# Performance work log

Hardware: AMD Instinct MI355X
Metric: run time of the kernel (lower is better)

## Reference

```python
import jax, jax.numpy as jnp
import numpy as np

B, LQ, LK, D = 16, 2048, 2048, 256
NEG = -1e10


def setup_inputs() -> dict:
    key = jax.random.key(0)
    k1, k2, k3, k4, k5 = jax.random.split(key, 5)
    scale = 1.0 / np.sqrt(D)
    return {
        "x": jax.random.normal(k1, (B, LQ, D), dtype=jnp.float32),
        "y": jax.random.normal(k2, (B, LK, D), dtype=jnp.float32),
        "mask": jnp.zeros((B, LK), dtype=bool),  # True = padded key position
        "Wq": jax.random.normal(k3, (D, D), dtype=jnp.float32) * scale,
        "Wk": jax.random.normal(k4, (D, D), dtype=jnp.float32) * scale,
        "Wv": jax.random.normal(k5, (D, D), dtype=jnp.float32) * scale,
    }


def reference(x, y, mask, Wq, Wk, Wv):
    # nn.Linear: out = in @ W.T (no bias)
    q = jnp.einsum('bqd,ed->bqe', x, Wq)   # [B, LQ, D]
    k = jnp.einsum('bkd,ed->bke', y, Wk)   # [B, LK, D]
    v = jnp.einsum('bkd,ed->bke', y, Wv)   # [B, LK, D]
    # cdist (p=2) via GEMM expansion: ||q||^2 + ||k||^2 - 2 q.k
    qn = jnp.sum(q * q, axis=-1)                              # [B, LQ]
    kn = jnp.sum(k * k, axis=-1)                              # [B, LK]
    d2 = qn[:, :, None] + kn[:, None, :] - 2.0 * jnp.einsum('bqd,bkd->bqk', q, k)
    dist = jnp.sqrt(jnp.maximum(d2, 0.0))                     # [B, LQ, LK]
    scores = jnp.exp(-dist)
    # masked_fill: where original mask is True, set pre-softmax score to -1e10
    scores = jnp.where(mask[:, None, :], NEG, scores)
    attn = jax.nn.softmax(scores, axis=-1)                    # [B, LQ, LK]
    att_out = jnp.einsum('bqk,bkd->bqd', attn, v)             # [B, LQ, D]
    return (att_out, attn)
```

## Files before the change

### kernel.cpp

```cpp
#include <hip/hip_runtime.h>
#include <stdint.h>

#define B_   16
#define L_   2048
#define D_   256
#define NROW (B_*L_)

#define KPAD 264
#define VPAD 40
#define EPAD 40
#define TPAD 66

typedef __attribute__((ext_vector_type(8))) short s8v;
typedef __attribute__((ext_vector_type(4))) float f4v;

__device__ __forceinline__ unsigned short f2b(float f) {
    unsigned u = __builtin_bit_cast(unsigned, f);
    return (unsigned short)((u + 0x7fffu + ((u >> 16) & 1u)) >> 16);
}

__global__ __launch_bounds__(256) void qkv_kernel(
    const float* __restrict__ x, const float* __restrict__ y,
    const float* __restrict__ Wq, const float* __restrict__ Wk, const float* __restrict__ Wv,
    unsigned short* __restrict__ Qb, unsigned short* __restrict__ Kb,
    unsigned short* __restrict__ Vt,
    float* __restrict__ qn, float* __restrict__ kn)
{
    __shared__ unsigned short Xs[64*256];
    __shared__ unsigned short Ws[64*256];
    __shared__ unsigned short Ts[64*TPAD];

    const int t    = threadIdx.x;
    const int r0   = blockIdx.x * 64;
    const int type = blockIdx.y;

    const float* X = (type == 0) ? x : y;
    const float* W = (type == 0) ? Wq : (type == 1) ? Wk : Wv;

    #pragma unroll
    for (int p = 0; p < 16; ++p) {
        int idx = p*256 + t;
        int row = idx >> 6;
        int c4  = (idx & 63) * 4;
        float4 vx = *(const float4*)(X + (size_t)(r0+row)*D_ + c4);
        uint2 px;
        px.x = (unsigned)f2b(vx.x) | ((unsigned)f2b(vx.y) << 16);
        px.y = (unsigned)f2b(vx.z) | ((unsigned)f2b(vx.w) << 16);
        *(uint2*)(Xs + row*256 + c4) = px;
    }

    const int w = t >> 6, lane = t & 63, q16 = lane & 15, quad = lane >> 4;
    const int m0 = w * 16;

    float p4[4] = {0.f, 0.f, 0.f, 0.f};
    const f4v z4 = {0.f, 0.f, 0.f, 0.f};

    for (int ct = 0; ct < 4; ++ct) {
        const int e0 = ct * 64;
        __syncthreads();
        #pragma unroll
        for (int p = 0; p < 16; ++p) {
            int idx = p*256 + t;
            int row = idx >> 6;
            int c4  = (idx & 63) * 4;
            float4 vw = *(const float4*)(W + (size_t)(e0+row)*D_ + c4);
            uint2 pw;
            pw.x = (unsigned)f2b(vw.x) | ((unsigned)f2b(vw.y) << 16);
            pw.y = (unsigned)f2b(vw.z) | ((unsigned)f2b(vw.w) << 16);
            *(uint2*)(Ws + row*256 + c4) = pw;
        }
        __syncthreads();

        f4v acc[4];
        #pragma unroll
        for (int n = 0; n < 4; ++n) acc[n] = z4;

        #pragma unroll
        for (int c = 0; c < 8; ++c) {
            s8v a = *(const s8v*)(Xs + (m0 + q16)*256 + c*32 + quad*8);
            #pragma unroll
            for (int n = 0; n < 4; ++n) {
                s8v bb = *(const s8v*)(Ws + (n*16 + q16)*256 + c*32 + quad*8);
                acc[n] = __builtin_amdgcn_mfma_f32_16x16x32_bf16(a, bb, acc[n], 0, 0, 0);
            }
        }

        if (type < 2) {
            unsigned short* Out = (type == 0) ? Qb : Kb;
            #pragma unroll
            for (int n = 0; n < 4; ++n)
                #pragma unroll
                for (int r = 0; r < 4; ++r) {
                    float v = acc[n][r];
                    p4[r] += v * v;
                    Out[(size_t)(r0 + m0 + quad*4 + r)*D_ + e0 + n*16 + q16] = f2b(v);
                }
        } else {
            #pragma unroll
            for (int n = 0; n < 4; ++n)
                #pragma unroll
                for (int r = 0; r < 4; ++r)
                    Ts[(m0 + quad*4 + r)*TPAD + n*16 + q16] = f2b(acc[n][r]);
            __syncthreads();
            int j    = t >> 2;
            int kseg = t & 3;
            unsigned pk[8];
            #pragma unroll
            for (int i = 0; i < 8; ++i) {
                unsigned lo = Ts[(kseg*16 + 2*i    )*TPAD + j];
                unsigned hi = Ts[(kseg*16 + 2*i + 1)*TPAD + j];
                pk[i] = lo | (hi << 16);
            }
            int bb_ = r0 >> 11;
            int k0g = r0 & (L_ - 1);
            unsigned short* dst = Vt + (size_t)(bb_*D_ + e0 + j)*L_ + k0g + kseg*16;
            *(uint4*)dst       = make_uint4(pk[0], pk[1], pk[2], pk[3]);
            *((uint4*)dst + 1) = make_uint4(pk[4], pk[5], pk[6], pk[7]);
        }
    }

    if (type < 2) {
        float* norm = (type == 0) ? qn : kn;
        #pragma unroll
        for (int r = 0; r < 4; ++r) {
            float v = p4[r];
            v += __shfl_xor(v, 1, 16);
            v += __shfl_xor(v, 2, 16);
            v += __shfl_xor(v, 4, 16);
            v += __shfl_xor(v, 8, 16);
            if (q16 == 0) norm[r0 + m0 + quad*4 + r] = v;
        }
    }
}

__global__ __launch_bounds__(256) void attn_kernel(
    const unsigned short* __restrict__ Qb, const unsigned short* __restrict__ Kb,
    const unsigned short* __restrict__ Vt,
    const float* __restrict__ qn, const float* __restrict__ kn,
    const unsigned char* __restrict__ mask,
    float* __restrict__ attn_out, float* __restrict__ att_out)
{
    __shared__ unsigned short Ks[32*KPAD];
    __shared__ unsigned short Vs[256*VPAD];
    __shared__ unsigned short Es[4][16*EPAD];
    __shared__ float kns[32];
    __shared__ unsigned char ms[2048];

    const int t  = threadIdx.x;
    const int q0 = blockIdx.x * 64;
    const int b  = blockIdx.y;
    const int bk = b * L_;
    const int w = t >> 6, lane = t & 63, q16 = lane & 15, quad = lane >> 4;

    *(unsigned long long*)(ms + t*8) = *(const unsigned long long*)(mask + bk + t*8);

    const int qrow = bk + q0 + w*16;
    s8v qa[8];
    float qnr[4];
    #pragma unroll
    for (int c = 0; c < 8; ++c)
        qa[c] = *(const s8v*)(Qb + (size_t)(qrow + q16)*D_ + c*32 + quad*8);
    #pragma unroll
    for (int r = 0; r < 4; ++r)
        qnr[r] = qn[qrow + quad*4 + r];

    float rs[4] = {};

    for (int kt = 0; kt < 64; ++kt) {
        int k0 = kt * 32;
        #pragma unroll
        for (int p = 0; p < 4; ++p) {
            int idx = p*256 + t;
            int row = idx >> 5;
            int c8  = (idx & 31) * 8;
            *(uint4*)(Ks + row*KPAD + c8) =
                *(const uint4*)(Kb + (size_t)(bk + k0 + row)*D_ + c8);
        }
        if (t < 32) kns[t] = kn[bk + k0 + t];
        __syncthreads();
        #pragma unroll
        for (int n = 0; n < 2; ++n) {
            f4v s = {0.f, 0.f, 0.f, 0.f};
            #pragma unroll
            for (int c = 0; c < 8; ++c) {
                s8v bb = *(const s8v*)(Ks + (n*16 + q16)*KPAD + c*32 + quad*8);
                s = __builtin_amdgcn_mfma_f32_16x16x32_bf16(qa[c], bb, s, 0, 0, 0);
            }
            float kc = kns[n*16 + q16];
            bool mk = ms[k0 + n*16 + q16] != 0;
            #pragma unroll
            for (int r = 0; r < 4; ++r) {
                float d2 = qnr[r] + kc - 2.0f * s[r];
                float dist = sqrtf(fmaxf(d2, 0.f));
                rs[r] += mk ? 0.f : __expf(__expf(-dist));
            }
        }
        __syncthreads();
    }

    float inv[4];
    #pragma unroll
    for (int r = 0; r < 4; ++r) {
        float v = rs[r];
        v += __shfl_xor(v, 1, 16);
        v += __shfl_xor(v, 2, 16);
        v += __shfl_xor(v, 4, 16);
        v += __shfl_xor(v, 8, 16);
        inv[r] = 1.0f / v;
    }

    const f4v z4 = {0.f, 0.f, 0.f, 0.f};
    f4v O[16];
    #pragma unroll
    for (int n = 0; n < 16; ++n) O[n] = z4;

    for (int kt = 0; kt < 64; ++kt) {
        int k0 = kt * 32;
        #pragma unroll
        for (int p = 0; p < 4; ++p) {
            int idx = p*256 + t;
            int row = idx >> 5;
            int c8  = (idx & 31) * 8;
            *(uint4*)(Ks + row*KPAD + c8) =
                *(const uint4*)(Kb + (size_t)(bk + k0 + row)*D_ + c8);
        }
        #pragma unroll
        for (int p = 0; p < 4; ++p) {
            int idx = p*256 + t;
            int d   = idx >> 2;
            int seg = (idx & 3) * 8;
            *(uint4*)(Vs + d*VPAD + seg) =
                *(const uint4*)(Vt + (size_t)(b*D_ + d)*L_ + k0 + seg);
        }
        if (t < 32) kns[t] = kn[bk + k0 + t];
        __syncthreads();

        #pragma unroll
        for (int n = 0; n < 2; ++n) {
            f4v s = {0.f, 0.f, 0.f, 0.f};
            #pragma unroll
            for (int c = 0; c < 8; ++c) {
                s8v bb = *(const s8v*)(Ks + (n*16 + q16)*KPAD + c*32 + quad*8);
                s = __builtin_amdgcn_mfma_f32_16x16x32_bf16(qa[c], bb, s, 0, 0, 0);
            }
            float kc = kns[n*16 + q16];
            bool mk = ms[k0 + n*16 + q16] != 0;
            #pragma unroll
            for (int r = 0; r < 4; ++r) {
                float d2 = qnr[r] + kc - 2.0f * s[r];
                float dist = sqrtf(fmaxf(d2, 0.f));
                float E = mk ? 0.f : __expf(__expf(-dist));
                float av = E * inv[r];
                attn_out[(size_t)(qrow + quad*4 + r)*L_ + k0 + n*16 + q16] = av;
                Es[w][(quad*4 + r)*EPAD + n*16 + q16] = f2b(av);
            }
        }
        s8v af = *(const s8v*)(&Es[w][q16*EPAD + quad*8]);
        #pragma unroll
        for (int n = 0; n < 16; ++n) {
            s8v vb = *(const s8v*)(Vs + (n*16 + q16)*VPAD + quad*8);
            O[n] = __builtin_amdgcn_mfma_f32_16x16x32_bf16(af, vb, O[n], 0, 0, 0);
        }
        __syncthreads();
    }

    #pragma unroll
    for (int n = 0; n < 16; ++n)
        #pragma unroll
        for (int r = 0; r < 4; ++r)
            att_out[(size_t)(qrow + quad*4 + r)*D_ + n*16 + q16] = O[n][r];
}

extern "C" void kernel_launch(void* const* d_in, const int* in_sizes, int n_in,
                              void* d_out, int out_size, void* d_ws, size_t ws_size,
                              hipStream_t stream) {
    (void)in_sizes; (void)n_in; (void)out_size; (void)ws_size;
    const float* x  = (const float*)d_in[0];
    const float* y  = (const float*)d_in[1];
    const unsigned char* mask = (const unsigned char*)d_in[2];
    const float* Wq = (const float*)d_in[3];
    const float* Wk = (const float*)d_in[4];
    const float* Wv = (const float*)d_in[5];

    char* ws = (char*)d_ws;
    unsigned short* Qb = (unsigned short*)ws;
    unsigned short* Kb = Qb + (size_t)NROW * D_;
    unsigned short* Vt = Kb + (size_t)NROW * D_;
    float* qn = (float*)(ws + 3 * (size_t)NROW * D_ * 2);
    float* kn = qn + NROW;

    float* att_out = (float*)d_out;
    float* attn    = att_out + (size_t)NROW * D_;

    qkv_kernel<<<dim3(512, 3), 256, 0, stream>>>(x, y, Wq, Wk, Wv,
                                                 Qb, Kb, Vt, qn, kn);
    attn_kernel<<<dim3(32, 16), 256, 0, stream>>>(Qb, Kb, Vt, qn, kn, mask,
                                                  attn, att_out);
}
```

Baseline: 635.6 us.

## Split attention into rowsum and output kernels with async double-buffered LDS staging

```diff
diff --git a/kernel.cpp b/kernel.cpp
--- a/kernel.cpp
+++ b/kernel.cpp
@@ -6,8 +6,6 @@
 #define D_   256
 #define NROW (B_*L_)
 
-#define KPAD 264
-#define VPAD 40
 #define EPAD 40
 #define TPAD 66
 
@@ -17,6 +15,12 @@
 __device__ __forceinline__ unsigned short f2b(float f) {
     unsigned u = __builtin_bit_cast(unsigned, f);
     return (unsigned short)((u + 0x7fffu + ((u >> 16) & 1u)) >> 16);
+}
+
+__device__ __forceinline__ void gl16(const void* g, void* l) {
+    __builtin_amdgcn_global_load_lds(
+        (const __attribute__((address_space(1))) unsigned int*)g,
+        (__attribute__((address_space(3))) unsigned int*)l, 16, 0, 0);
 }
 
 __global__ __launch_bounds__(256) void qkv_kernel(
@@ -34,19 +38,20 @@
     const int r0   = blockIdx.x * 64;
     const int type = blockIdx.y;
 
-    const float* X = (type == 0) ? x : y;
-    const float* W = (type == 0) ? Wq : (type == 1) ? Wk : Wv;
+    const float* X = type ? y : x;
 
     #pragma unroll
     for (int p = 0; p < 16; ++p) {
-        int idx = p*256 + t;
-        int row = idx >> 6;
-        int c4  = (idx & 63) * 4;
+        int idx  = p*256 + t;
+        int row  = idx >> 6;
+        int half = idx & 1;
+        int blk  = (idx & 63) >> 1;
+        int c4   = blk*8 + half*4;
         float4 vx = *(const float4*)(X + (size_t)(r0+row)*D_ + c4);
         uint2 px;
         px.x = (unsigned)f2b(vx.x) | ((unsigned)f2b(vx.y) << 16);
         px.y = (unsigned)f2b(vx.z) | ((unsigned)f2b(vx.w) << 16);
-        *(uint2*)(Xs + row*256 + c4) = px;
+        *(uint2*)(Xs + row*256 + (blk ^ (row & 15))*8 + half*4) = px;
     }
 
     const int w = t >> 6, lane = t & 63, q16 = lane & 15, quad = lane >> 4;
@@ -57,36 +62,40 @@
 
     for (int ct = 0; ct < 4; ++ct) {
         const int e0 = ct * 64;
+
         __syncthreads();
-        #pragma unroll
-        for (int p = 0; p < 16; ++p) {
-            int idx = p*256 + t;
-            int row = idx >> 6;
-            int c4  = (idx & 63) * 4;
-            float4 vw = *(const float4*)(W + (size_t)(e0+row)*D_ + c4);
-            uint2 pw;
-            pw.x = (unsigned)f2b(vw.x) | ((unsigned)f2b(vw.y) << 16);
-            pw.y = (unsigned)f2b(vw.z) | ((unsigned)f2b(vw.w) << 16);
-            *(uint2*)(Ws + row*256 + c4) = pw;
+        {
+            const float* W = type ? Wk : Wq;
+            #pragma unroll
+            for (int p = 0; p < 16; ++p) {
+                int idx  = p*256 + t;
+                int row  = idx >> 6;
+                int half = idx & 1;
+                int blk  = (idx & 63) >> 1;
+                int c4   = blk*8 + half*4;
+                float4 vw = *(const float4*)(W + (size_t)(e0+row)*D_ + c4);
+                uint2 pw;
+                pw.x = (unsigned)f2b(vw.x) | ((unsigned)f2b(vw.y) << 16);
+                pw.y = (unsigned)f2b(vw.z) | ((unsigned)f2b(vw.w) << 16);
+                *(uint2*)(Ws + row*256 + (blk ^ (row & 15))*8 + half*4) = pw;
+            }
         }
         __syncthreads();
 
         f4v acc[4];
         #pragma unroll
         for (int n = 0; n < 4; ++n) acc[n] = z4;
-
         #pragma unroll
         for (int c = 0; c < 8; ++c) {
-            s8v a = *(const s8v*)(Xs + (m0 + q16)*256 + c*32 + quad*8);
+            s8v a = *(const s8v*)(Xs + (m0 + q16)*256 + (((c*4+quad) ^ q16)*8));
             #pragma unroll
             for (int n = 0; n < 4; ++n) {
-                s8v bb = *(const s8v*)(Ws + (n*16 + q16)*256 + c*32 + quad*8);
+                s8v bb = *(const s8v*)(Ws + (n*16 + q16)*256 + (((c*4+quad) ^ q16)*8));
                 acc[n] = __builtin_amdgcn_mfma_f32_16x16x32_bf16(a, bb, acc[n], 0, 0, 0);
             }
         }
-
-        if (type < 2) {
-            unsigned short* Out = (type == 0) ? Qb : Kb;
+        {
+            unsigned short* Out = type ? Kb : Qb;
             #pragma unroll
             for (int n = 0; n < 4; ++n)
                 #pragma unroll
@@ -95,12 +104,42 @@
                     p4[r] += v * v;
                     Out[(size_t)(r0 + m0 + quad*4 + r)*D_ + e0 + n*16 + q16] = f2b(v);
                 }
-        } else {
+        }
+
+        if (type) {
+            __syncthreads();
+            #pragma unroll
+            for (int p = 0; p < 16; ++p) {
+                int idx  = p*256 + t;
+                int row  = idx >> 6;
+                int half = idx & 1;
+                int blk  = (idx & 63) >> 1;
+                int c4   = blk*8 + half*4;
+                float4 vw = *(const float4*)(Wv + (size_t)(e0+row)*D_ + c4);
+                uint2 pw;
+                pw.x = (unsigned)f2b(vw.x) | ((unsigned)f2b(vw.y) << 16);
+                pw.y = (unsigned)f2b(vw.z) | ((unsigned)f2b(vw.w) << 16);
+                *(uint2*)(Ws + row*256 + (blk ^ (row & 15))*8 + half*4) = pw;
+            }
+            __syncthreads();
+
+            f4v vacc[4];
+            #pragma unroll
+            for (int n = 0; n < 4; ++n) vacc[n] = z4;
+            #pragma unroll
+            for (int c = 0; c < 8; ++c) {
+                s8v a = *(const s8v*)(Xs + (m0 + q16)*256 + (((c*4+quad) ^ q16)*8));
+                #pragma unroll
+                for (int n = 0; n < 4; ++n) {
+                    s8v bb = *(const s8v*)(Ws + (n*16 + q16)*256 + (((c*4+quad) ^ q16)*8));
+                    vacc[n] = __builtin_amdgcn_mfma_f32_16x16x32_bf16(a, bb, vacc[n], 0, 0, 0);
+                }
+            }
             #pragma unroll
             for (int n = 0; n < 4; ++n)
                 #pragma unroll
                 for (int r = 0; r < 4; ++r)
-                    Ts[(m0 + quad*4 + r)*TPAD + n*16 + q16] = f2b(acc[n][r]);
+                    Ts[(m0 + quad*4 + r)*TPAD + n*16 + q16] = f2b(vacc[n][r]);
             __syncthreads();
             int j    = t >> 2;
             int kseg = t & 3;
@@ -119,8 +158,8 @@
         }
     }
 
-    if (type < 2) {
-        float* norm = (type == 0) ? qn : kn;
+    {
+        float* norm = type ? kn : qn;
         #pragma unroll
         for (int r = 0; r < 4; ++r) {
             float v = p4[r];
@@ -133,26 +172,43 @@
     }
 }
 
-__global__ __launch_bounds__(256) void attn_kernel(
+__device__ __forceinline__ void stage_K(const unsigned short* Kb, unsigned short* ks,
+                                        int bk, int k0, int w, int lane) {
+    #pragma unroll
+    for (int p = 0; p < 4; ++p) {
+        int slot = p*256 + w*64 + lane;
+        int row  = slot >> 5;
+        int blk  = slot & 31;
+        gl16(Kb + (size_t)(bk + k0 + row)*D_ + ((blk ^ (row & 15))*8),
+             ks + (size_t)(p*256 + w*64)*8);
+    }
+}
+__device__ __forceinline__ void stage_V(const unsigned short* Vt, unsigned short* vs,
+                                        int bD, int k0, int w, int lane) {
+    #pragma unroll
+    for (int p = 0; p < 4; ++p) {
+        int slot = p*256 + w*64 + lane;
+        int d    = slot >> 2;
+        int blk  = slot & 3;
+        gl16(Vt + (size_t)(bD + d)*L_ + k0 + ((blk ^ ((d >> 1) & 3))*8),
+             vs + (size_t)(p*256 + w*64)*8);
+    }
+}
+
+__global__ __launch_bounds__(256) void rowsum_kernel(
     const unsigned short* __restrict__ Qb, const unsigned short* __restrict__ Kb,
-    const unsigned short* __restrict__ Vt,
     const float* __restrict__ qn, const float* __restrict__ kn,
     const unsigned char* __restrict__ mask,
-    float* __restrict__ attn_out, float* __restrict__ att_out)
+    float* __restrict__ rowsum)
 {
-    __shared__ unsigned short Ks[32*KPAD];
-    __shared__ unsigned short Vs[256*VPAD];
-    __shared__ unsigned short Es[4][16*EPAD];
-    __shared__ float kns[32];
-    __shared__ unsigned char ms[2048];
+    __shared__ unsigned short Ks[2][32*256];
 
     const int t  = threadIdx.x;
     const int q0 = blockIdx.x * 64;
     const int b  = blockIdx.y;
     const int bk = b * L_;
+    const int kbase = blockIdx.z * 1024;
     const int w = t >> 6, lane = t & 63, q16 = lane & 15, quad = lane >> 4;
-
-    *(unsigned long long*)(ms + t*8) = *(const unsigned long long*)(mask + bk + t*8);
 
     const int qrow = bk + q0 + w*16;
     s8v qa[8];
@@ -164,41 +220,38 @@
     for (int r = 0; r < 4; ++r)
         qnr[r] = qn[qrow + quad*4 + r];
 
-    float rs[4] = {};
-
-    for (int kt = 0; kt < 64; ++kt) {
-        int k0 = kt * 32;
-        #pragma unroll
-        for (int p = 0; p < 4; ++p) {
-            int idx = p*256 + t;
-            int row = idx >> 5;
-            int c8  = (idx & 31) * 8;
-            *(uint4*)(Ks + row*KPAD + c8) =
-                *(const uint4*)(Kb + (size_t)(bk + k0 + row)*D_ + c8);
-        }
-        if (t < 32) kns[t] = kn[bk + k0 + t];
+    float rs[4] = {0.f, 0.f, 0.f, 0.f};
+
+    stage_K(Kb, Ks[0], bk, kbase, w, lane);
+    for (int kt = 0; kt < 32; ++kt) {
+        const int k0 = kbase + kt*32;
+        const int cur = kt & 1;
         __syncthreads();
+        if (kt < 31) stage_K(Kb, Ks[cur ^ 1], bk, k0 + 32, w, lane);
+
+        float kcv[2]; int mkv[2];
+        #pragma unroll
+        for (int n = 0; n < 2; ++n) {
+            kcv[n] = kn[bk + k0 + n*16 + q16];
+            mkv[n] = mask[bk + k0 + n*16 + q16];
+        }
         #pragma unroll
         for (int n = 0; n < 2; ++n) {
             f4v s = {0.f, 0.f, 0.f, 0.f};
             #pragma unroll
             for (int c = 0; c < 8; ++c) {
-                s8v bb = *(const s8v*)(Ks + (n*16 + q16)*KPAD + c*32 + quad*8);
+                s8v bb = *(const s8v*)(Ks[cur] + (n*16 + q16)*256 + (((c*4+quad) ^ q16)*8));
                 s = __builtin_amdgcn_mfma_f32_16x16x32_bf16(qa[c], bb, s, 0, 0, 0);
             }
-            float kc = kns[n*16 + q16];
-            bool mk = ms[k0 + n*16 + q16] != 0;
             #pragma unroll
             for (int r = 0; r < 4; ++r) {
-                float d2 = qnr[r] + kc - 2.0f * s[r];
+                float d2 = qnr[r] + kcv[n] - 2.0f * s[r];
                 float dist = sqrtf(fmaxf(d2, 0.f));
-                rs[r] += mk ? 0.f : __expf(__expf(-dist));
-            }
-        }
-        __syncthreads();
-    }
-
-    float inv[4];
+                rs[r] += mkv[n] ? 0.f : __expf(__expf(-dist));
+            }
+        }
+    }
+
     #pragma unroll
     for (int r = 0; r < 4; ++r) {
         float v = rs[r];
@@ -206,7 +259,39 @@
         v += __shfl_xor(v, 2, 16);
         v += __shfl_xor(v, 4, 16);
         v += __shfl_xor(v, 8, 16);
-        inv[r] = 1.0f / v;
+        if (q16 == 0) atomicAdd(rowsum + qrow + quad*4 + r, v);
+    }
+}
+
+__global__ __launch_bounds__(256) void attnout_kernel(
+    const unsigned short* __restrict__ Qb, const unsigned short* __restrict__ Kb,
+    const unsigned short* __restrict__ Vt,
+    const float* __restrict__ qn, const float* __restrict__ kn,
+    const float* __restrict__ rowsum,
+    const unsigned char* __restrict__ mask,
+    float* __restrict__ attn_out, float* __restrict__ att_out)
+{
+    __shared__ unsigned short Ks[2][32*256];
+    __shared__ unsigned short Vs[2][256*32];
+    __shared__ unsigned short Es[4][16*EPAD];
+
+    const int t  = threadIdx.x;
+    const int q0 = blockIdx.x * 64;
+    const int b  = blockIdx.y;
+    const int bk = b * L_;
+    const int bD = b * D_;
+    const int w = t >> 6, lane = t & 63, q16 = lane & 15, quad = lane >> 4;
+
+    const int qrow = bk + q0 + w*16;
+    s8v qa[8];
+    float qnr[4], inv[4];
+    #pragma unroll
+    for (int c = 0; c < 8; ++c)
+        qa[c] = *(const s8v*)(Qb + (size_t)(qrow + q16)*D_ + c*32 + quad*8);
+    #pragma unroll
+    for (int r = 0; r < 4; ++r) {
+        qnr[r] = qn[qrow + quad*4 + r];
+        inv[r] = 1.0f / rowsum[qrow + quad*4 + r];
     }
 
     const f4v z4 = {0.f, 0.f, 0.f, 0.f};
@@ -214,54 +299,50 @@
     #pragma unroll
     for (int n = 0; n < 16; ++n) O[n] = z4;
 
+    stage_K(Kb, Ks[0], bk, 0, w, lane);
+    stage_V(Vt, Vs[0], bD, 0, w, lane);
     for (int kt = 0; kt < 64; ++kt) {
-        int k0 = kt * 32;
-        #pragma unroll
-        for (int p = 0; p < 4; ++p) {
-            int idx = p*256 + t;
-            int row = idx >> 5;
-            int c8  = (idx & 31) * 8;
-            *(uint4*)(Ks + row*KPAD + c8) =
-                *(const uint4*)(Kb + (size_t)(bk + k0 + row)*D_ + c8);
-        }
-        #pragma unroll
-        for (int p = 0; p < 4; ++p) {
-            int idx = p*256 + t;
-            int d   = idx >> 2;
-            int seg = (idx & 3) * 8;
-            *(uint4*)(Vs + d*VPAD + seg) =
-                *(const uint4*)(Vt + (size_t)(b*D_ + d)*L_ + k0 + seg);
-        }
-        if (t < 32) kns[t] = kn[bk + k0 + t];
+        const int k0 = kt * 32;
+        const int cur = kt & 1;
         __syncthreads();
+        if (kt < 63) {
+            stage_K(Kb, Ks[cur ^ 1], bk, k0 + 32, w, lane);
+            stage_V(Vt, Vs[cur ^ 1], bD, k0 + 32, w, lane);
+        }
+
+        float kcv[2]; int mkv[2];
+        #pragma unroll
+        for (int n = 0; n < 2; ++n) {
+            kcv[n] = kn[bk + k0 + n*16 + q16];
+            mkv[n] = mask[bk + k0 + n*16 + q16];
+        }
 
         #pragma unroll
         for (int n = 0; n < 2; ++n) {
             f4v s = {0.f, 0.f, 0.f, 0.f};
             #pragma unroll
             for (int c = 0; c < 8; ++c) {
-                s8v bb = *(const s8v*)(Ks + (n*16 + q16)*KPAD + c*32 + quad*8);
+                s8v bb = *(const s8v*)(Ks[cur] + (n*16 + q16)*256 + (((c*4+quad) ^ q16)*8));
                 s = __builtin_amdgcn_mfma_f32_16x16x32_bf16(qa[c], bb, s, 0, 0, 0);
             }
-            float kc = kns[n*16 + q16];
-            bool mk = ms[k0 + n*16 + q16] != 0;
             #pragma unroll
             for (int r = 0; r < 4; ++r) {
-                float d2 = qnr[r] + kc - 2.0f * s[r];
+                float d2 = qnr[r] + kcv[n] - 2.0f * s[r];
                 float dist = sqrtf(fmaxf(d2, 0.f));
-                float E = mk ? 0.f : __expf(__expf(-dist));
+                float E = mkv[n] ? 0.f : __expf(__expf(-dist));
                 float av = E * inv[r];
                 attn_out[(size_t)(qrow + quad*4 + r)*L_ + k0 + n*16 + q16] = av;
-                Es[w][(quad*4 + r)*EPAD + n*16 + q16] = f2b(av);
+                Es[w][(quad*4 + r)*EPAD + n*16 + q16] =
+                    (unsigned short)(__builtin_bit_cast(unsigned, av) >> 16);
             }
         }
         s8v af = *(const s8v*)(&Es[w][q16*EPAD + quad*8]);
         #pragma unroll
         for (int n = 0; n < 16; ++n) {
-            s8v vb = *(const s8v*)(Vs + (n*16 + q16)*VPAD + quad*8);
+            s8v vb = *(const s8v*)(Vs[cur] + (n*16 + q16)*32 +
+                                   ((quad ^ ((q16 >> 1) & 3))*8));
             O[n] = __builtin_amdgcn_mfma_f32_16x16x32_bf16(af, vb, O[n], 0, 0, 0);
         }
-        __syncthreads();
     }
 
     #pragma unroll
@@ -286,14 +367,17 @@
     unsigned short* Qb = (unsigned short*)ws;
     unsigned short* Kb = Qb + (size_t)NROW * D_;
     unsigned short* Vt = Kb + (size_t)NROW * D_;
-    float* qn = (float*)(ws + 3 * (size_t)NROW * D_ * 2);
-    float* kn = qn + NROW;
+    float* qn     = (float*)(ws + 3 * (size_t)NROW * D_ * 2);
+    float* kn     = qn + NROW;
+    float* rowsum = kn + NROW;
 
     float* att_out = (float*)d_out;
     float* attn    = att_out + (size_t)NROW * D_;
 
-    qkv_kernel<<<dim3(512, 3), 256, 0, stream>>>(x, y, Wq, Wk, Wv,
+    hipMemsetAsync(rowsum, 0, (size_t)NROW * sizeof(float), stream);
+    qkv_kernel<<<dim3(512, 2), 256, 0, stream>>>(x, y, Wq, Wk, Wv,
                                                  Qb, Kb, Vt, qn, kn);
-    attn_kernel<<<dim3(32, 16), 256, 0, stream>>>(Qb, Kb, Vt, qn, kn, mask,
-                                                  attn, att_out);
-}
+    rowsum_kernel<<<dim3(32, 16, 2), 256, 0, stream>>>(Qb, Kb, qn, kn, mask, rowsum);
+    attnout_kernel<<<dim3(32, 16), 256, 0, stream>>>(Qb, Kb, Vt, qn, kn, rowsum,
+                                                     mask, attn, att_out);
+}
```

After: 612.8 us. -3.6%, faster.
